# Kernel tuning notes

Measured on AMD Instinct MI355X. Metric: run time of the kernel, lower is better.

The kernel has to match this reference:

```python
import jax, jax.numpy as jnp
import numpy as np

H = 768; B = 8; T = 1024; V = 50257
S = 256      # token_distribution_samples
K = 64       # token_topk
POOL = 1024  # max(S*4, K) token pool
TEMP = 0.1; LIM = 0.25; MW = 0.1


def _ln(x, g, b):
    m = x.mean(-1, keepdims=True)
    v = ((x - m) ** 2).mean(-1, keepdims=True)
    return (x - m) / jnp.sqrt(v + 1e-5) * g + b


def _head(x, g, b, w1, b1, w2, b2):
    # LayerNorm -> Linear -> GELU(exact) -> (Dropout=identity in eval) -> Linear
    h = _ln(x, g, b) @ w1 + b1
    h = jax.nn.gelu(h, approximate=False)
    return h @ w2 + b2


def _l2norm(x):
    return x / jnp.maximum(jnp.linalg.norm(x, axis=-1, keepdims=True), 1e-12)


def setup_inputs() -> dict:
    key = jax.random.key(0)
    ks = jax.random.split(key, 16)
    init = lambda k, shp: jax.random.normal(k, shp, jnp.float32) * 0.02
    f32 = jnp.float32
    return {
        "latent": jax.random.normal(ks[0], (B, T, H), f32),
        "token_embedding_matrix": jax.random.normal(ks[1], (V, H), f32),
        # scale head
        "scale_ln_g": jnp.ones((H,), f32), "scale_ln_b": jnp.zeros((H,), f32),
        "scale_w1": init(ks[2], (H, H)), "scale_b1": jnp.zeros((H,), f32),
        "scale_w2": init(ks[3], (H, H)), "scale_b2": jnp.zeros((H,), f32),
        # bias head
        "bias_ln_g": jnp.ones((H,), f32), "bias_ln_b": jnp.zeros((H,), f32),
        "bias_w1": init(ks[4], (H, H)), "bias_b1": jnp.zeros((H,), f32),
        "bias_w2": init(ks[5], (H, H)), "bias_b2": jnp.zeros((H,), f32),
        # contrastive head (projection_dim == H)
        "con_ln_g": jnp.ones((H,), f32), "con_ln_b": jnp.zeros((H,), f32),
        "con_w1": init(ks[6], (H, H)), "con_b1": jnp.zeros((H,), f32),
        "con_w2": init(ks[7], (H, H)), "con_b2": jnp.zeros((H,), f32),
        # deterministic augmentation noise (randn_like * 0.01)
        "noise_a": jax.random.normal(ks[8], (B * T, H), f32) * 0.01,
        "noise_b": jax.random.normal(ks[9], (B * T, H), f32) * 0.01,
        # deterministic row-sampling (torch.randperm analogues)
        "samp_idx": jax.random.permutation(ks[10], B * T)[:S].astype(jnp.int32),
        "tok_idx": jax.random.permutation(ks[11], V)[:POOL].astype(jnp.int32),
    }


def reference(latent, token_embedding_matrix,
              scale_ln_g, scale_ln_b, scale_w1, scale_b1, scale_w2, scale_b2,
              bias_ln_g, bias_ln_b, bias_w1, bias_b1, bias_w2, bias_b2,
              con_ln_g, con_ln_b, con_w1, con_b1, con_w2, con_b2,
              noise_a, noise_b, samp_idx, tok_idx):
    # compensate: u = s(z)*z + b(z)
    scale = 1.0 + LIM * jnp.tanh(_head(latent, scale_ln_g, scale_ln_b, scale_w1, scale_b1, scale_w2, scale_b2))
    bias = LIM * jnp.tanh(_head(latent, bias_ln_g, bias_ln_b, bias_w1, bias_b1, bias_w2, bias_b2))
    aligned = scale * latent + bias

    flat = aligned.reshape(-1, H)  # [N, H], N = B*T
    # contrastive loss
    va = _l2norm(_head(flat + noise_a, con_ln_g, con_ln_b, con_w1, con_b1, con_w2, con_b2))
    vb = _l2norm(_head(flat + noise_b, con_ln_g, con_ln_b, con_w1, con_b1, con_w2, con_b2))
    logits = va @ vb.T / TEMP  # [N, N]
    loss_ab = -jnp.mean(jnp.diagonal(jax.nn.log_softmax(logits, axis=-1)))
    loss_ba = -jnp.mean(jnp.diagonal(jax.nn.log_softmax(logits.T, axis=-1)))
    con_loss = 0.5 * (loss_ab + loss_ba)

    # token distribution loss
    af = flat[samp_idx]                     # [S, H]
    te = token_embedding_matrix[tok_idx]    # [POOL, H]
    tl = _l2norm(af) @ _l2norm(te).T / TEMP  # [S, POOL]
    top_vals, top_idx = jax.lax.top_k(tl, K)
    top_emb = te[top_idx]                   # [S, K, H] gather
    w = jax.nn.softmax(top_vals, axis=-1)[..., None]
    proto = (w * top_emb).sum(axis=1)       # [S, H]
    proto_loss = jnp.mean((af - proto) ** 2)
    moment_loss = jnp.mean((af.mean(0) - te.mean(0)) ** 2) \
        + jnp.mean((af.std(0) - te.std(0)) ** 2)
    token_dist_loss = proto_loss + MW * moment_loss

    comp_reg_loss = jnp.mean((scale - 1.0) ** 2) + jnp.mean(bias ** 2)
    return (aligned, con_loss, token_dist_loss, comp_reg_loss, scale, bias)
```

## Files before the change

kernel.cpp:

```cpp
#include <hip/hip_runtime.h>
#include <hip/hip_bf16.h>

typedef __hip_bfloat16 bf16;
typedef __attribute__((ext_vector_type(4))) float f32x4;
typedef __attribute__((ext_vector_type(8))) short bf16x8v;

static constexpr int   HD    = 768;
static constexpr int   NRr   = 8192;
static constexpr int   SSAMP = 256;
static constexpr int   KTOP  = 64;
static constexpr int   NPOOL = 1024;
static constexpr float TINV  = 10.0f;

__device__ __forceinline__ float bf2f(bf16 h){ return __bfloat162float(h); }
__device__ __forceinline__ bf16  f2bf(float f){ return __float2bfloat16(f); }

__device__ __forceinline__ float gelu_exact(float x){
  return 0.5f * x * (1.0f + erff(x * 0.70710678118654752f));
}

__device__ __forceinline__ float block_sum(float v, float* buf){
  const int lane = threadIdx.x & 63, w = threadIdx.x >> 6;
  const int nw = (int)blockDim.x >> 6;
  #pragma unroll
  for(int o = 32; o; o >>= 1) v += __shfl_down(v, o);
  __syncthreads();
  if(lane == 0) buf[w] = v;
  __syncthreads();
  float t = 0.f;
  for(int i = 0; i < nw; i++) t += buf[i];
  return t;
}

__device__ __forceinline__ void gload_lds16(const bf16* g, bf16* lds_uniform){
  __builtin_amdgcn_global_load_lds(
      (const __attribute__((address_space(1))) unsigned int*)(const void*)g,
      (__attribute__((address_space(3))) unsigned int*)(void*)lds_uniform,
      16, 0, 0);
}

struct TsA { const float* w[6]; const float* gg[6]; bf16* o[6]; };
__global__ __launch_bounds__(256)
void tscale6(TsA a){
  __shared__ float t[32][33];
  const int z = blockIdx.z;
  const float* Win = a.w[z];
  const float* g   = a.gg[z];
  bf16* Wt         = a.o[z];
  const int tx = threadIdx.x, ty = threadIdx.y;
  const int bx = blockIdx.x * 32, by = blockIdx.y * 32;
  #pragma unroll
  for(int j = 0; j < 4; j++)
    t[ty + j*8][tx] = Win[(size_t)(by + ty + j*8) * HD + bx + tx];
  __syncthreads();
  const float gv = g ? g[by + tx] : 1.0f;
  #pragma unroll
  for(int j = 0; j < 4; j++)
    Wt[(size_t)(bx + ty + j*8) * HD + by + tx] = f2bf(gv * t[tx][ty + j*8]);
}

struct FbA { const float* bln[3]; const float* w1[3]; const float* b1[3]; float* o[3]; };
__global__ __launch_bounds__(256)
void foldbias3(FbA a){
  __shared__ float red[4][64];
  const int h = blockIdx.y;
  const int lane = threadIdx.x & 63, w = threadIdx.x >> 6;
  const int n = blockIdx.x * 64 + lane;
  const float* bl = a.bln[h];
  const float* w1 = a.w1[h];
  float t = 0.f;
  for(int k = w * 192; k < w * 192 + 192; k++)
    t += bl[k] * w1[(size_t)k * HD + n];
  red[w][lane] = t;
  __syncthreads();
  if(w == 0)
    a.o[h][n] = a.b1[h][n] + red[0][lane] + red[1][lane] + red[2][lane] + red[3][lane];
}

__global__ __launch_bounds__(256)
void lnxh_kernel(const float* __restrict__ x, const float* __restrict__ na,
                 const float* __restrict__ nb, bf16* __restrict__ o){
  __shared__ float buf[4];
  const int row = blockIdx.x, tid = threadIdx.x;
  const float* noise = nullptr;
  if(na) noise = (row < NRr) ? na : nb;
  const size_t srow = (size_t)(row & (NRr - 1)) * HD;
  const size_t nrow = noise ? ((size_t)(row & (NRr - 1)) * HD) : 0;
  const size_t drow = (size_t)row * HD;
  float v[3];
  #pragma unroll
  for(int j = 0; j < 3; j++){
    const int i = tid + j*256;
    float t = x[srow + i];
    if(noise) t += noise[nrow + i];
    v[j] = t;
  }
  float s = v[0] + v[1] + v[2];
  s = block_sum(s, buf);
  const float m = s * (1.0f / HD);
  float q = 0.f;
  #pragma unroll
  for(int j = 0; j < 3; j++){ const float d = v[j] - m; q += d*d; }
  q = block_sum(q, buf);
  const float inv = rsqrtf(q * (1.0f / HD) + 1e-5f);
  #pragma unroll
  for(int j = 0; j < 3; j++)
    o[drow + tid + j*256] = f2bf((v[j] - m) * inv);
}

enum { EPI_GELU = 0, EPI_SB = 1, EPI_RAW = 3, EPI_LOGITS = 4, EPI_TL = 5 };

template<int EPI>
__global__ __launch_bounds__(256, 2)
void gemm_kernel(const bf16* __restrict__ A, const bf16* __restrict__ Bt,
                 const bf16* __restrict__ Bt2,
                 const int M, const int N, const int K,
                 const int lda, const int ldc,
                 const float* __restrict__ bias, const float* __restrict__ bias2,
                 bf16* __restrict__ outb, float* __restrict__ outf,
                 float* __restrict__ outf2,
                 float* __restrict__ aux, float* __restrict__ aux2){
  __shared__ __align__(16) bf16 As[128 * 32];
  __shared__ __align__(16) bf16 Bs[128 * 32];
  __shared__ float rbuf[512];

  const int tid  = threadIdx.x;
  const int wave = tid >> 6, lane = tid & 63;
  const int wm = wave >> 1, wn = wave & 1;
  const int r16 = lane & 15, kh = lane >> 4;
  const int bx = blockIdx.x, by = blockIdx.y;
  const int row0 = by * 128, col0 = bx * 128;

  float addv = 0.f;
  if constexpr(EPI == EPI_SB){
    if(blockIdx.z == 0){ addv = 1.0f; }
    else { A += 768; Bt = Bt2; bias = bias2; outf = outf2; }
  }

  f32x4 acc[4][4];
  #pragma unroll
  for(int i = 0; i < 4; i++)
    #pragma unroll
    for(int j = 0; j < 4; j++){ f32x4 z = {0.f,0.f,0.f,0.f}; acc[i][j] = z; }

  const int c0 = tid, c1 = tid + 256;
  const int r0c = c0 >> 2, p0 = c0 & 3;
  const int r1c = c1 >> 2, p1 = c1 & 3;
  const int g0 = (p0 - ((r0c >> 1) & 3)) & 3;
  const int g1 = (p1 - ((r1c >> 1) & 3)) & 3;
  const bf16* gA0 = A  + (size_t)(row0 + r0c) * lda + g0 * 8;
  const bf16* gA1 = A  + (size_t)(row0 + r1c) * lda + g1 * 8;
  const bf16* gB0 = Bt + (size_t)(col0 + r0c) * K + g0 * 8;
  const bf16* gB1 = Bt + (size_t)(col0 + r1c) * K + g1 * 8;
  bf16* lA0 = As + (wave * 64) * 8;
  bf16* lA1 = As + (256 + wave * 64) * 8;
  bf16* lB0 = Bs + (wave * 64) * 8;
  bf16* lB1 = Bs + (256 + wave * 64) * 8;

  const int sA = (r16 >> 1) & 3;
  const int kphys = ((kh + sA) & 3) * 8;

  for(int k0 = 0; k0 < K; k0 += 32){
    __syncthreads();
    gload_lds16(gA0 + k0, lA0);
    gload_lds16(gA1 + k0, lA1);
    gload_lds16(gB0 + k0, lB0);
    gload_lds16(gB1 + k0, lB1);
    __syncthreads();
    bf16x8v av[4], bv[4];
    #pragma unroll
    for(int f = 0; f < 4; f++){
      av[f] = *(const bf16x8v*)(As + (wm*64 + f*16 + r16) * 32 + kphys);
      bv[f] = *(const bf16x8v*)(Bs + (wn*64 + f*16 + r16) * 32 + kphys);
    }
    #pragma unroll
    for(int i = 0; i < 4; i++)
      #pragma unroll
      for(int j = 0; j < 4; j++)
        acc[i][j] = __builtin_amdgcn_mfma_f32_16x16x32_bf16(av[i], bv[j], acc[i][j], 0, 0, 0);
  }

  const int crow0 = row0 + wm * 64;
  const int ccol0 = col0 + wn * 64;

  if constexpr(EPI != EPI_LOGITS){
    float part = 0.f;
    #pragma unroll
    for(int i = 0; i < 4; i++){
      #pragma unroll
      for(int j = 0; j < 4; j++){
        const int col = ccol0 + j*16 + r16;
        const float bvv = bias ? bias[col] : 0.f;
        #pragma unroll
        for(int q = 0; q < 4; q++){
          const int row = crow0 + i*16 + kh*4 + q;
          const float v = acc[i][j][q] + bvv;
          const size_t off = (size_t)row * ldc + col;
          if constexpr(EPI == EPI_GELU){
            outb[off] = f2bf(gelu_exact(v));
          } else if constexpr(EPI == EPI_SB){
            const float t = 0.25f * tanhf(v);
            outf[off] = t + addv;
            part += t * t;
          } else if constexpr(EPI == EPI_TL){
            outf[off] = v * TINV;
          } else {
            outb[off] = f2bf(v);
          }
        }
      }
    }
    if constexpr(EPI == EPI_SB){
      const float tot2 = block_sum(part, rbuf);
      if(tid == 0)
        aux[(size_t)blockIdx.z * (gridDim.x * gridDim.y) + by * gridDim.x + bx] = tot2;
    }
  } else {
    float rs[16], cs[4];
    #pragma unroll
    for(int t = 0; t < 16; t++) rs[t] = 0.f;
    #pragma unroll
    for(int t = 0; t < 4; t++) cs[t] = 0.f;
    #pragma unroll
    for(int i = 0; i < 4; i++)
      #pragma unroll
      for(int j = 0; j < 4; j++)
        #pragma unroll
        for(int q = 0; q < 4; q++){
          const float ev = expf(acc[i][j][q] * TINV);
          rs[i*4 + q] += ev;
          cs[j]       += ev;
        }
    #pragma unroll
    for(int t = 0; t < 16; t++){
      float r = rs[t];
      r += __shfl_xor(r, 1); r += __shfl_xor(r, 2);
      r += __shfl_xor(r, 4); r += __shfl_xor(r, 8);
      rs[t] = r;
    }
    if(r16 == 0){
      #pragma unroll
      for(int i = 0; i < 4; i++)
        #pragma unroll
        for(int q = 0; q < 4; q++)
          rbuf[wn*128 + wm*64 + i*16 + kh*4 + q] = rs[i*4 + q];
    }
    #pragma unroll
    for(int j = 0; j < 4; j++){
      float c = cs[j];
      c += __shfl_xor(c, 16); c += __shfl_xor(c, 32);
      cs[j] = c;
    }
    if(kh == 0){
      #pragma unroll
      for(int j = 0; j < 4; j++)
        rbuf[256 + wm*128 + wn*64 + j*16 + r16] = cs[j];
    }
    __syncthreads();
    if(tid < 128){
      aux [(size_t)bx * M + row0 + tid] = rbuf[tid]       + rbuf[128 + tid];
      aux2[(size_t)by * M + col0 + tid] = rbuf[256 + tid] + rbuf[384 + tid];
    }
  }
}

__global__ __launch_bounds__(256)
void aligned_kernel(const float* __restrict__ latent, const float* __restrict__ sc,
                    const float* __restrict__ bi, float* __restrict__ outp){
  const size_t i4 = ((size_t)blockIdx.x * 256 + threadIdx.x) * 4;
  const float4 l = *(const float4*)(latent + i4);
  float4 o;
  o.x = sc[i4+0] * l.x + bi[i4+0];
  o.y = sc[i4+1] * l.y + bi[i4+1];
  o.z = sc[i4+2] * l.z + bi[i4+2];
  o.w = sc[i4+3] * l.w + bi[i4+3];
  *(float4*)(outp + i4) = o;
}

__global__ __launch_bounds__(256)
void l2n_kernel(bf16* __restrict__ vio){
  __shared__ float buf[4];
  const int row = blockIdx.x, tid = threadIdx.x;
  const size_t base = (size_t)row * HD;
  float v[3];
  #pragma unroll
  for(int j = 0; j < 3; j++) v[j] = bf2f(vio[base + tid + j*256]);
  float q = v[0]*v[0] + v[1]*v[1] + v[2]*v[2];
  q = block_sum(q, buf);
  const float inv = 1.0f / fmaxf(sqrtf(q), 1e-12f);
  #pragma unroll
  for(int j = 0; j < 3; j++) vio[base + tid + j*256] = f2bf(v[j] * inv);
}

__global__ __launch_bounds__(256)
void diag_kernel(const bf16* __restrict__ va, const bf16* __restrict__ vb,
                 float* __restrict__ diag){
  const int lane = threadIdx.x & 63;
  const int row = blockIdx.x * 4 + (threadIdx.x >> 6);
  const size_t base = (size_t)row * HD;
  float d = 0.f;
  #pragma unroll
  for(int j = 0; j < 12; j++){
    const int i = lane + j*64;
    d += bf2f(va[base + i]) * bf2f(vb[base + i]);
  }
  #pragma unroll
  for(int o = 32; o; o >>= 1) d += __shfl_down(d, o);
  if(lane == 0) diag[row] = d * TINV;
}

__global__ __launch_bounds__(256)
void rcsum_kernel(const float* __restrict__ rp, const float* __restrict__ cp,
                  float* __restrict__ rs, float* __restrict__ cs, const int nb){
  const int i = blockIdx.x * 256 + threadIdx.x;
  float r = 0.f, c = 0.f;
  for(int b = 0; b < nb; b++){
    r += rp[(size_t)b * NRr + i];
    c += cp[(size_t)b * NRr + i];
  }
  rs[i] = r; cs[i] = c;
}

__global__ __launch_bounds__(256)
void af_kernel(const float* __restrict__ aligned, const int* __restrict__ samp,
               float* __restrict__ afraw, bf16* __restrict__ afn){
  __shared__ float buf[4];
  const int s = blockIdx.x, tid = threadIdx.x;
  const size_t src = (size_t)samp[s] * HD, dst = (size_t)s * HD;
  float v[3];
  #pragma unroll
  for(int j = 0; j < 3; j++){
    const int i = tid + j*256;
    v[j] = aligned[src + i];
    afraw[dst + i] = v[j];
  }
  float q = v[0]*v[0] + v[1]*v[1] + v[2]*v[2];
  q = block_sum(q, buf);
  const float inv = 1.0f / fmaxf(sqrtf(q), 1e-12f);
  #pragma unroll
  for(int j = 0; j < 3; j++) afn[dst + tid + j*256] = f2bf(v[j] * inv);
}

__global__ __launch_bounds__(256)
void te_kernel(const float* __restrict__ emb, const int* __restrict__ tok,
               float* __restrict__ teg, bf16* __restrict__ ten){
  __shared__ float buf[4];
  const int p = blockIdx.x, tid = threadIdx.x;
  const size_t src = (size_t)tok[p] * HD, dst = (size_t)p * HD;
  float v[3];
  #pragma unroll
  for(int j = 0; j < 3; j++){
    const int i = tid + j*256;
    v[j] = emb[src + i];
    teg[dst + i] = v[j];
  }
  float q = v[0]*v[0] + v[1]*v[1] + v[2]*v[2];
  q = block_sum(q, buf);
  const float inv = 1.0f / fmaxf(sqrtf(q), 1e-12f);
  #pragma unroll
  for(int j = 0; j < 3; j++) ten[dst + tid + j*256] = f2bf(v[j] * inv);
}

__global__ __launch_bounds__(256)
void topk_kernel(const float* __restrict__ tl, const float* __restrict__ teg,
                 const float* __restrict__ afraw, float* __restrict__ protopart){
  __shared__ float sv[NPOOL];
  __shared__ float topv[KTOP];
  __shared__ int   topi[KTOP];
  __shared__ float wts[KTOP];
  __shared__ float rv[4];
  __shared__ int   ri[4];
  __shared__ float buf[4];
  __shared__ float sinv;
  const int s = blockIdx.x, tid = threadIdx.x;
  const int lane = tid & 63, w = tid >> 6;
  #pragma unroll
  for(int j = 0; j < 4; j++) sv[tid + j*256] = tl[(size_t)s * NPOOL + tid + j*256];
  __syncthreads();
  for(int k = 0; k < KTOP; k++){
    float bvv = -1e30f; int bi = 0x7fffffff;
    #pragma unroll
    for(int j = 0; j < 4; j++){
      const int i = tid + j*256;
      const float x = sv[i];
      if(x > bvv || (x == bvv && i < bi)){ bvv = x; bi = i; }
    }
    #pragma unroll
    for(int o = 1; o < 64; o <<= 1){
      const float ov = __shfl_xor(bvv, o);
      const int   oi = __shfl_xor(bi, o);
      if(ov > bvv || (ov == bvv && oi < bi)){ bvv = ov; bi = oi; }
    }
    if(lane == 0){ rv[w] = bvv; ri[w] = bi; }
    __syncthreads();
    if(tid == 0){
      for(int w2 = 1; w2 < 4; w2++)
        if(rv[w2] > bvv || (rv[w2] == bvv && ri[w2] < bi)){ bvv = rv[w2]; bi = ri[w2]; }
      if(bi < 0 || bi >= NPOOL) bi = 0;
      topv[k] = bvv; topi[k] = bi; sv[bi] = -1e30f;
    }
    __syncthreads();
  }
  if(tid < KTOP) wts[tid] = expf(topv[tid] - topv[0]);
  __syncthreads();
  if(tid == 0){
    float t = 0.f;
    for(int k = 0; k < KTOP; k++) t += wts[k];
    sinv = 1.0f / t;
  }
  __syncthreads();
  float part = 0.f;
  #pragma unroll
  for(int j = 0; j < 3; j++){
    const int h = tid + j*256;
    float ph = 0.f;
    for(int k = 0; k < KTOP; k++) ph += wts[k] * teg[(size_t)topi[k] * HD + h];
    ph *= sinv;
    const float d = afraw[(size_t)s * HD + h] - ph;
    part += d * d;
  }
  part = block_sum(part, buf);
  if(tid == 0) protopart[s] = part;
}

__global__ __launch_bounds__(768)
void mom1_kernel(const float* __restrict__ afraw, const float* __restrict__ teg,
                 float* __restrict__ partial){
  const int b = blockIdx.x, h = threadIdx.x;
  float sa = 0.f, sa2 = 0.f, st = 0.f, st2 = 0.f;
  for(int r = b * 40; r < b * 40 + 40; r++){
    if(r < SSAMP){
      const float v = afraw[(size_t)r * HD + h];
      sa += v; sa2 += v * v;
    } else {
      const float v = teg[(size_t)(r - SSAMP) * HD + h];
      st += v; st2 += v * v;
    }
  }
  partial[(size_t)(b*4 + 0) * HD + h] = sa;
  partial[(size_t)(b*4 + 1) * HD + h] = sa2;
  partial[(size_t)(b*4 + 2) * HD + h] = st;
  partial[(size_t)(b*4 + 3) * HD + h] = st2;
}

__global__ __launch_bounds__(768)
void mom2_kernel(const float* __restrict__ partial, float* __restrict__ mom){
  __shared__ float buf[12];
  const int h = threadIdx.x;
  float sa = 0.f, sa2 = 0.f, st = 0.f, st2 = 0.f;
  for(int b = 0; b < 32; b++){
    sa  += partial[(size_t)(b*4 + 0) * HD + h];
    sa2 += partial[(size_t)(b*4 + 1) * HD + h];
    st  += partial[(size_t)(b*4 + 2) * HD + h];
    st2 += partial[(size_t)(b*4 + 3) * HD + h];
  }
  const float ma  = sa * (1.0f / SSAMP);
  const float sda = sqrtf(fmaxf(sa2 * (1.0f / SSAMP) - ma * ma, 0.f));
  const float mt  = st * (1.0f / NPOOL);
  const float sdt = sqrtf(fmaxf(st2 * (1.0f / NPOOL) - mt * mt, 0.f));
  const float dmu = ma - mt, dsd = sda - sdt;
  const float t1 = block_sum(dmu * dmu, buf);
  const float t2 = block_sum(dsd * dsd, buf);
  if(h == 0){ mom[0] = t1; mom[1] = t2; }
}

__global__ __launch_bounds__(1024)
void final_kernel(const float* __restrict__ rs, const float* __restrict__ cs,
                  const float* __restrict__ diag,
                  const float* __restrict__ aux, const int naux,
                  const float* __restrict__ protopart, const float* __restrict__ mom,
                  float* __restrict__ outsc){
  __shared__ float buf[16];
  const int tid = threadIdx.x;
  float s1 = 0.f, s2 = 0.f;
  for(int r = tid; r < NRr; r += 1024){
    const float dg = diag[r];
    s1 += logf(rs[r]) - dg;
    s2 += logf(cs[r]) - dg;
  }
  float c1 = 0.f;
  for(int j = tid; j < naux; j += 1024) c1 += aux[j];
  float pp = 0.f;
  for(int j = tid; j < SSAMP; j += 1024) pp += protopart[j];
  s1 = block_sum(s1, buf);
  s2 = block_sum(s2, buf);
  c1 = block_sum(c1, buf);
  pp = block_sum(pp, buf);
  if(tid == 0){
    const float con  = 0.5f * (s1 + s2) / (float)NRr;
    const float creg = c1 / 6291456.0f;
    const float tdl  = pp / (float)(SSAMP * HD) + 0.1f * ((mom[0] + mom[1]) / (float)HD);
    outsc[0] = con;
    outsc[1] = tdl;
    outsc[2] = creg;
  }
}

extern "C" void kernel_launch(void* const* d_in, const int* in_sizes, int n_in,
                              void* d_out, int out_size, void* d_ws, size_t ws_size,
                              hipStream_t stream){
  (void)in_sizes; (void)n_in; (void)out_size; (void)ws_size;
  const float* latent = (const float*)d_in[0];
  const float* tokemb = (const float*)d_in[1];
  const float* s_g  = (const float*)d_in[2];  const float* s_bln = (const float*)d_in[3];
  const float* s_w1 = (const float*)d_in[4];  const float* s_b1  = (const float*)d_in[5];
  const float* s_w2 = (const float*)d_in[6];  const float* s_b2  = (const float*)d_in[7];
  const float* b_g  = (const float*)d_in[8];  const float* b_bln = (const float*)d_in[9];
  const float* b_w1 = (const float*)d_in[10]; const float* b_b1  = (const float*)d_in[11];
  const float* b_w2 = (const float*)d_in[12]; const float* b_b2  = (const float*)d_in[13];
  const float* c_g  = (const float*)d_in[14]; const float* c_bln = (const float*)d_in[15];
  const float* c_w1 = (const float*)d_in[16]; const float* c_b1  = (const float*)d_in[17];
  const float* c_w2 = (const float*)d_in[18]; const float* c_b2  = (const float*)d_in[19];
  const float* noise_a = (const float*)d_in[20];
  const float* noise_b = (const float*)d_in[21];
  const int*  samp = (const int*)d_in[22];
  const int*  tok  = (const int*)d_in[23];

  float* out = (float*)d_out;
  float* out_aligned = out;
  float* out_scalars = out + (size_t)NRr * HD;
  float* out_scale   = out + (size_t)NRr * HD + 3;
  float* out_bias    = out_scale + (size_t)NRr * HD;

  char* wp = (char*)d_ws;
  auto alloc = [&](size_t bytes) -> char* {
    char* p = wp; wp += (bytes + 255) & ~(size_t)255; return p;
  };
  bf16* wt_comb1 = (bf16*)alloc((size_t)2*HD*HD*2);
  bf16* wt_c1    = (bf16*)alloc((size_t)HD*HD*2);
  bf16* wt_s2    = (bf16*)alloc((size_t)HD*HD*2);
  bf16* wt_b2    = (bf16*)alloc((size_t)HD*HD*2);
  bf16* wt_c2    = (bf16*)alloc((size_t)HD*HD*2);
  float* bcomb1  = (float*)alloc(2*HD*4);
  float* bc1     = (float*)alloc(HD*4);
  bf16* A1 = (bf16*)alloc((size_t)2*NRr*HD*2);
  bf16* A2 = (bf16*)alloc((size_t)2*NRr*HD*2);
  float* rowpart = (float*)alloc((size_t)64*NRr*4);
  float* colpart = (float*)alloc((size_t)64*NRr*4);
  float* rowsum  = (float*)alloc((size_t)NRr*4);
  float* colsum  = (float*)alloc((size_t)NRr*4);
  float* diag    = (float*)alloc((size_t)NRr*4);
  float* aux     = (float*)alloc(768*4);
  float* afraw   = (float*)alloc((size_t)SSAMP*HD*4);
  float* teg     = (float*)alloc((size_t)NPOOL*HD*4);
  float* tlb     = (float*)alloc((size_t)SSAMP*NPOOL*4);
  float* protopart = (float*)alloc(SSAMP*4);
  float* mom     = (float*)alloc(2*4);
  float* mompart = rowpart;
  bf16*  ten     = (bf16*)colpart;
  bf16*  afn     = (bf16*)(colpart + ((size_t)NPOOL*HD*2)/4);

  TsA ts;
  ts.w[0]=s_w1; ts.gg[0]=s_g;     ts.o[0]=wt_comb1;
  ts.w[1]=b_w1; ts.gg[1]=b_g;     ts.o[1]=wt_comb1 + (size_t)HD*HD;
  ts.w[2]=c_w1; ts.gg[2]=c_g;     ts.o[2]=wt_c1;
  ts.w[3]=s_w2; ts.gg[3]=nullptr; ts.o[3]=wt_s2;
  ts.w[4]=b_w2; ts.gg[4]=nullptr; ts.o[4]=wt_b2;
  ts.w[5]=c_w2; ts.gg[5]=nullptr; ts.o[5]=wt_c2;
  tscale6<<<dim3(24,24,6), dim3(32,8), 0, stream>>>(ts);
  FbA fb;
  fb.bln[0]=s_bln; fb.w1[0]=s_w1; fb.b1[0]=s_b1; fb.o[0]=bcomb1;
  fb.bln[1]=b_bln; fb.w1[1]=b_w1; fb.b1[1]=b_b1; fb.o[1]=bcomb1 + HD;
  fb.bln[2]=c_bln; fb.w1[2]=c_w1; fb.b1[2]=c_b1; fb.o[2]=bc1;
  foldbias3<<<dim3(12,3), 256, 0, stream>>>(fb);

  lnxh_kernel<<<NRr, 256, 0, stream>>>(latent, nullptr, nullptr, A2);
  gemm_kernel<EPI_GELU><<<dim3(12,64), 256, 0, stream>>>(
      A2, wt_comb1, nullptr, NRr, 2*HD, HD, HD, 2*HD, bcomb1, nullptr,
      A1, nullptr, nullptr, nullptr, nullptr);
  gemm_kernel<EPI_SB><<<dim3(6,64,2), 256, 0, stream>>>(
      A1, wt_s2, wt_b2, NRr, HD, HD, 2*HD, HD, s_b2, b_b2,
      nullptr, out_scale, out_bias, aux, nullptr);
  aligned_kernel<<<(NRr * HD) / (256 * 4), 256, 0, stream>>>(latent, out_scale, out_bias, out_aligned);

  lnxh_kernel<<<2*NRr, 256, 0, stream>>>(out_aligned, noise_a, noise_b, A1);
  gemm_kernel<EPI_GELU><<<dim3(6,128), 256, 0, stream>>>(
      A1, wt_c1, nullptr, 2*NRr, HD, HD, HD, HD, bc1, nullptr,
      A2, nullptr, nullptr, nullptr, nullptr);
  gemm_kernel<EPI_RAW><<<dim3(6,128), 256, 0, stream>>>(
      A2, wt_c2, nullptr, 2*NRr, HD, HD, HD, HD, c_b2, nullptr,
      A1, nullptr, nullptr, nullptr, nullptr);
  l2n_kernel<<<2*NRr, 256, 0, stream>>>(A1);
  bf16* va = A1;
  bf16* vb = A1 + (size_t)NRr * HD;

  gemm_kernel<EPI_LOGITS><<<dim3(64,64), 256, 0, stream>>>(
      va, vb, nullptr, NRr, NRr, HD, HD, 0, nullptr, nullptr,
      nullptr, nullptr, nullptr, rowpart, colpart);
  rcsum_kernel<<<NRr / 256, 256, 0, stream>>>(rowpart, colpart, rowsum, colsum, 64);
  diag_kernel<<<NRr / 4, 256, 0, stream>>>(va, vb, diag);

  af_kernel<<<SSAMP, 256, 0, stream>>>(out_aligned, samp, afraw, afn);
  te_kernel<<<NPOOL, 256, 0, stream>>>(tokemb, tok, teg, ten);
  gemm_kernel<EPI_TL><<<dim3(8,2), 256, 0, stream>>>(
      afn, ten, nullptr, SSAMP, NPOOL, HD, HD, NPOOL, nullptr, nullptr,
      nullptr, tlb, nullptr, nullptr, nullptr);
  topk_kernel<<<SSAMP, 256, 0, stream>>>(tlb, teg, afraw, protopart);
  mom1_kernel<<<32, 768, 0, stream>>>(afraw, teg, mompart);
  mom2_kernel<<<1, 768, 0, stream>>>(mompart, mom);

  final_kernel<<<1, 1024, 0, stream>>>(rowsum, colsum, diag, aux, 768,
                                       protopart, mom, out_scalars);
}
```

Before: 547.7 us.

## Double GEMM K-tile to 64 and fuse aligned computation with noisy layernorm

The GEMM main loop now stages a 64-wide K slice per iteration instead of 32, using an 8-way XOR swizzle and two MFMA sub-steps per barrier pair. This halves the number of synchronisation rounds per tile, at the cost of doubling LDS per block, which may reduce occupancy. Separately, the aligned elementwise kernel and the two noisy layernorm passes are merged into one kernel. It computes aligned once, writes it, and normalises both noise variants from registers, avoiding re-reading aligned and the extra launches.

```diff
diff --git a/kernel.cpp b/kernel.cpp
--- a/kernel.cpp
+++ b/kernel.cpp
@@ -30,6 +30,19 @@
   float t = 0.f;
   for(int i = 0; i < nw; i++) t += buf[i];
   return t;
+}
+
+__device__ __forceinline__ void block_sum2(float& a, float& b, float* buf){
+  const int lane = threadIdx.x & 63, w = threadIdx.x >> 6;
+  #pragma unroll
+  for(int o = 32; o; o >>= 1){ a += __shfl_down(a, o); b += __shfl_down(b, o); }
+  __syncthreads();
+  if(lane == 0){ buf[w] = a; buf[4 + w] = b; }
+  __syncthreads();
+  float ta = 0.f, tb = 0.f;
+  #pragma unroll
+  for(int i = 0; i < 4; i++){ ta += buf[i]; tb += buf[4 + i]; }
+  a = ta; b = tb;
 }
 
 __device__ __forceinline__ void gload_lds16(const bf16* g, bf16* lds_uniform){
@@ -78,23 +91,13 @@
 }
 
 __global__ __launch_bounds__(256)
-void lnxh_kernel(const float* __restrict__ x, const float* __restrict__ na,
-                 const float* __restrict__ nb, bf16* __restrict__ o){
+void lnxh_kernel(const float* __restrict__ x, bf16* __restrict__ o){
   __shared__ float buf[4];
   const int row = blockIdx.x, tid = threadIdx.x;
-  const float* noise = nullptr;
-  if(na) noise = (row < NRr) ? na : nb;
-  const size_t srow = (size_t)(row & (NRr - 1)) * HD;
-  const size_t nrow = noise ? ((size_t)(row & (NRr - 1)) * HD) : 0;
-  const size_t drow = (size_t)row * HD;
+  const size_t base = (size_t)row * HD;
   float v[3];
   #pragma unroll
-  for(int j = 0; j < 3; j++){
-    const int i = tid + j*256;
-    float t = x[srow + i];
-    if(noise) t += noise[nrow + i];
-    v[j] = t;
-  }
+  for(int j = 0; j < 3; j++) v[j] = x[base + tid + j*256];
   float s = v[0] + v[1] + v[2];
   s = block_sum(s, buf);
   const float m = s * (1.0f / HD);
@@ -105,7 +108,45 @@
   const float inv = rsqrtf(q * (1.0f / HD) + 1e-5f);
   #pragma unroll
   for(int j = 0; j < 3; j++)
-    o[drow + tid + j*256] = f2bf((v[j] - m) * inv);
+    o[base + tid + j*256] = f2bf((v[j] - m) * inv);
+}
+
+__global__ __launch_bounds__(256)
+void fuse_al_ln(const float* __restrict__ latent, const float* __restrict__ sc,
+                const float* __restrict__ bi, const float* __restrict__ na,
+                const float* __restrict__ nb, float* __restrict__ out_aligned,
+                bf16* __restrict__ X){
+  __shared__ float buf[8];
+  const int row = blockIdx.x, tid = threadIdx.x;
+  const size_t base = (size_t)row * HD;
+  float ua[3], ub[3];
+  #pragma unroll
+  for(int j = 0; j < 3; j++){
+    const int i = tid + j*256;
+    const float a = sc[base + i] * latent[base + i] + bi[base + i];
+    out_aligned[base + i] = a;
+    ua[j] = a + na[base + i];
+    ub[j] = a + nb[base + i];
+  }
+  float sa = ua[0] + ua[1] + ua[2];
+  float sb = ub[0] + ub[1] + ub[2];
+  block_sum2(sa, sb, buf);
+  const float ma = sa * (1.0f / HD), mb = sb * (1.0f / HD);
+  float qa = 0.f, qb = 0.f;
+  #pragma unroll
+  for(int j = 0; j < 3; j++){
+    const float da = ua[j] - ma; qa += da*da;
+    const float db = ub[j] - mb; qb += db*db;
+  }
+  block_sum2(qa, qb, buf);
+  const float ia = rsqrtf(qa * (1.0f / HD) + 1e-5f);
+  const float ib = rsqrtf(qb * (1.0f / HD) + 1e-5f);
+  #pragma unroll
+  for(int j = 0; j < 3; j++){
+    const int i = tid + j*256;
+    X[base + i] = f2bf((ua[j] - ma) * ia);
+    X[(size_t)(row + NRr) * HD + i] = f2bf((ub[j] - mb) * ib);
+  }
 }
 
 enum { EPI_GELU = 0, EPI_SB = 1, EPI_RAW = 3, EPI_LOGITS = 4, EPI_TL = 5 };
@@ -120,8 +161,8 @@
                  bf16* __restrict__ outb, float* __restrict__ outf,
                  float* __restrict__ outf2,
                  float* __restrict__ aux, float* __restrict__ aux2){
-  __shared__ __align__(16) bf16 As[128 * 32];
-  __shared__ __align__(16) bf16 Bs[128 * 32];
+  __shared__ __align__(16) bf16 As[128 * 64];
+  __shared__ __align__(16) bf16 Bs[128 * 64];
   __shared__ float rbuf[512];
 
   const int tid  = threadIdx.x;
@@ -143,41 +184,43 @@
     #pragma unroll
     for(int j = 0; j < 4; j++){ f32x4 z = {0.f,0.f,0.f,0.f}; acc[i][j] = z; }
 
-  const int c0 = tid, c1 = tid + 256;
-  const int r0c = c0 >> 2, p0 = c0 & 3;
-  const int r1c = c1 >> 2, p1 = c1 & 3;
-  const int g0 = (p0 - ((r0c >> 1) & 3)) & 3;
-  const int g1 = (p1 - ((r1c >> 1) & 3)) & 3;
-  const bf16* gA0 = A  + (size_t)(row0 + r0c) * lda + g0 * 8;
-  const bf16* gA1 = A  + (size_t)(row0 + r1c) * lda + g1 * 8;
-  const bf16* gB0 = Bt + (size_t)(col0 + r0c) * K + g0 * 8;
-  const bf16* gB1 = Bt + (size_t)(col0 + r1c) * K + g1 * 8;
-  bf16* lA0 = As + (wave * 64) * 8;
-  bf16* lA1 = As + (256 + wave * 64) * 8;
-  bf16* lB0 = Bs + (wave * 64) * 8;
-  bf16* lB1 = Bs + (256 + wave * 64) * 8;
-
-  const int sA = (r16 >> 1) & 3;
-  const int kphys = ((kh + sA) & 3) * 8;
-
-  for(int k0 = 0; k0 < K; k0 += 32){
+  const bf16* gA[4]; const bf16* gB[4];
+  bf16* lA[4]; bf16* lB[4];
+  #pragma unroll
+  for(int j = 0; j < 4; j++){
+    const int c = tid + j*256;
+    const int rr = c >> 3, p = c & 7;
+    const int g = (p - (rr & 7)) & 7;
+    gA[j] = A  + (size_t)(row0 + rr) * lda + g * 8;
+    gB[j] = Bt + (size_t)(col0 + rr) * K   + g * 8;
+    lA[j] = As + ((size_t)j*256 + wave*64) * 8;
+    lB[j] = Bs + ((size_t)j*256 + wave*64) * 8;
+  }
+  const int sw = r16 & 7;
+
+  for(int k0 = 0; k0 < K; k0 += 64){
     __syncthreads();
-    gload_lds16(gA0 + k0, lA0);
-    gload_lds16(gA1 + k0, lA1);
-    gload_lds16(gB0 + k0, lB0);
-    gload_lds16(gB1 + k0, lB1);
+    #pragma unroll
+    for(int j = 0; j < 4; j++){
+      gload_lds16(gA[j] + k0, lA[j]);
+      gload_lds16(gB[j] + k0, lB[j]);
+    }
     __syncthreads();
-    bf16x8v av[4], bv[4];
-    #pragma unroll
-    for(int f = 0; f < 4; f++){
-      av[f] = *(const bf16x8v*)(As + (wm*64 + f*16 + r16) * 32 + kphys);
-      bv[f] = *(const bf16x8v*)(Bs + (wn*64 + f*16 + r16) * 32 + kphys);
-    }
-    #pragma unroll
-    for(int i = 0; i < 4; i++)
+    #pragma unroll
+    for(int kk = 0; kk < 2; kk++){
+      const int koff = ((kk*4 + kh + sw) & 7) * 8;
+      bf16x8v av[4], bv[4];
       #pragma unroll
-      for(int j = 0; j < 4; j++)
-        acc[i][j] = __builtin_amdgcn_mfma_f32_16x16x32_bf16(av[i], bv[j], acc[i][j], 0, 0, 0);
+      for(int f = 0; f < 4; f++){
+        av[f] = *(const bf16x8v*)(As + (wm*64 + f*16 + r16) * 64 + koff);
+        bv[f] = *(const bf16x8v*)(Bs + (wn*64 + f*16 + r16) * 64 + koff);
+      }
+      #pragma unroll
+      for(int i = 0; i < 4; i++)
+        #pragma unroll
+        for(int j = 0; j < 4; j++)
+          acc[i][j] = __builtin_amdgcn_mfma_f32_16x16x32_bf16(av[i], bv[j], acc[i][j], 0, 0, 0);
+    }
   }
 
   const int crow0 = row0 + wm * 64;
@@ -262,19 +305,6 @@
       aux2[(size_t)by * M + col0 + tid] = rbuf[256 + tid] + rbuf[384 + tid];
     }
   }
-}
-
-__global__ __launch_bounds__(256)
-void aligned_kernel(const float* __restrict__ latent, const float* __restrict__ sc,
-                    const float* __restrict__ bi, float* __restrict__ outp){
-  const size_t i4 = ((size_t)blockIdx.x * 256 + threadIdx.x) * 4;
-  const float4 l = *(const float4*)(latent + i4);
-  float4 o;
-  o.x = sc[i4+0] * l.x + bi[i4+0];
-  o.y = sc[i4+1] * l.y + bi[i4+1];
-  o.z = sc[i4+2] * l.z + bi[i4+2];
-  o.w = sc[i4+3] * l.w + bi[i4+3];
-  *(float4*)(outp + i4) = o;
 }
 
 __global__ __launch_bounds__(256)
@@ -564,16 +594,17 @@
   fb.bln[2]=c_bln; fb.w1[2]=c_w1; fb.b1[2]=c_b1; fb.o[2]=bc1;
   foldbias3<<<dim3(12,3), 256, 0, stream>>>(fb);
 
-  lnxh_kernel<<<NRr, 256, 0, stream>>>(latent, nullptr, nullptr, A2);
+  lnxh_kernel<<<NRr, 256, 0, stream>>>(latent, A2);
   gemm_kernel<EPI_GELU><<<dim3(12,64), 256, 0, stream>>>(
       A2, wt_comb1, nullptr, NRr, 2*HD, HD, HD, 2*HD, bcomb1, nullptr,
       A1, nullptr, nullptr, nullptr, nullptr);
   gemm_kernel<EPI_SB><<<dim3(6,64,2), 256, 0, stream>>>(
       A1, wt_s2, wt_b2, NRr, HD, HD, 2*HD, HD, s_b2, b_b2,
       nullptr, out_scale, out_bias, aux, nullptr);
-  aligned_kernel<<<(NRr * HD) / (256 * 4), 256, 0, stream>>>(latent, out_scale, out_bias, out_aligned);
-
-  lnxh_kernel<<<2*NRr, 256, 0, stream>>>(out_aligned, noise_a, noise_b, A1);
+
+  fuse_al_ln<<<NRr, 256, 0, stream>>>(latent, out_scale, out_bias,
+                                      noise_a, noise_b, out_aligned, A1);
+
   gemm_kernel<EPI_GELU><<<dim3(6,128), 256, 0, stream>>>(
       A1, wt_c1, nullptr, 2*NRr, HD, HD, HD, HD, bc1, nullptr,
       A2, nullptr, nullptr, nullptr, nullptr);
```

Measured after the change: 518.1 us. -5.4%, faster.
